# Optimization experiments

Hardware: AMD Instinct MI355X
Metric: run time of the kernel (lower is better)

The kernel has to match this reference:

```python
import jax, jax.numpy as jnp
import numpy as np

B, N, K, H, Cin, Cout = 2, 8192, 16, 4, 64, 128
D = Cout // H  # head_dim = 32


def setup_inputs() -> dict:
    key = jax.random.key(0)
    ks = jax.random.split(key, 16)
    x = jax.random.normal(ks[0], (B, N, Cin), jnp.float32)
    pos = jax.random.uniform(ks[1], (B, N, 3), jnp.float32)
    # KNN indices (torch.no_grad in original): pairwise squared distance + top_k
    sq = jnp.sum(pos * pos, -1)
    d2 = sq[:, :, None] - 2.0 * jnp.einsum('bnc,bmc->bnm', pos, pos) + sq[:, None, :]
    _, idx = jax.lax.top_k(-d2, K)  # (B, N, K) int32

    def lin(k, fin, fout):
        kw, kb = jax.random.split(k)
        lim = 1.0 / np.sqrt(fin)
        W = jax.random.uniform(kw, (fin, fout), jnp.float32, -lim, lim)
        b = jax.random.uniform(kb, (fout,), jnp.float32, -lim, lim)
        return W, b

    Wq, bq = lin(ks[2], Cin, Cout)
    Wkv, bkv = lin(ks[3], Cin, 2 * Cout)
    Wp1, bp1 = lin(ks[4], 3, Cout)
    Wp2, bp2 = lin(ks[5], Cout, Cout)
    Wa1, ba1 = lin(ks[6], Cout, Cout)
    Wa2, ba2 = lin(ks[7], Cout, Cout)
    Wo, bo = lin(ks[8], Cout, Cout)
    return dict(x=x, pos=pos, idx=idx, Wq=Wq, bq=bq, Wkv=Wkv, bkv=bkv,
                Wp1=Wp1, bp1=bp1, Wp2=Wp2, bp2=bp2,
                Wa1=Wa1, ba1=ba1, Wa2=Wa2, ba2=ba2, Wo=Wo, bo=bo)


def reference(x, pos, idx, Wq, bq, Wkv, bkv, Wp1, bp1, Wp2, bp2,
              Wa1, ba1, Wa2, ba2, Wo, bo):
    q = (x @ Wq + bq).reshape(B, N, H, D)
    kv = x @ Wkv + bkv
    k, v = kv[..., :Cout].reshape(B, N, H, D), kv[..., Cout:].reshape(B, N, H, D)
    bix = jnp.arange(B)[:, None, None]
    pos_n = pos[bix, idx]          # (B,N,K,3)
    k_n = k[bix, idx]              # (B,N,K,H,D)
    v_n = v[bix, idx]              # (B,N,K,H,D)
    pos_diff = pos[:, :, None, :] - pos_n
    pos_enc = jax.nn.relu(pos_diff @ Wp1 + bp1) @ Wp2 + bp2   # (B,N,K,Cout)
    pos_enc_h = pos_enc.reshape(B, N, K, H, D)
    rel = (k_n - q[:, :, None] + pos_enc_h).reshape(B, N, K, Cout)
    attn = jax.nn.relu(rel @ Wa1 + ba1) @ Wa2 + ba2           # (B,N,K,Cout)
    attn = jax.nn.softmax(attn.reshape(B, N, K, H, D), axis=2)
    agg = jnp.sum(attn * (v_n + pos_enc_h), axis=2).reshape(B, N, Cout)
    return agg @ Wo + bo
```

## Files before the change

kernel.cpp:

```cpp
#include <hip/hip_runtime.h>
#include <stdint.h>


typedef __attribute__((ext_vector_type(8))) short short8;
typedef __attribute__((ext_vector_type(4))) float f32x4;
typedef __attribute__((ext_vector_type(4))) unsigned int u32x4;

#define NN_TOT 16384
#define PES 136

__device__ __forceinline__ uint32_t pk_bf16(float a, float b) {
  uint32_t r;
  asm("v_cvt_pk_bf16_f32 %0, %1, %2" : "=v"(r) : "v"(a), "v"(b));
  return r;
}
__device__ __forceinline__ float lo_f(uint32_t p) {
  return __builtin_bit_cast(float, p << 16);
}
__device__ __forceinline__ float hi_f(uint32_t p) {
  return __builtin_bit_cast(float, p & 0xffff0000u);
}
__device__ __forceinline__ short f2bf_rne(float f) {
  uint32_t u = __builtin_bit_cast(uint32_t, f);
  uint32_t r = (u + 0x7FFFu + ((u >> 16) & 1u)) >> 16;
  return (short)r;
}
__device__ __forceinline__ float bf2f(unsigned short s) {
  uint32_t u = ((uint32_t)s) << 16;
  return __builtin_bit_cast(float, u);
}

__global__ __launch_bounds__(256) void prep_frags(
    const float* __restrict__ Wq, const float* __restrict__ Wkv,
    const float* __restrict__ Wp2, const float* __restrict__ Wa1,
    const float* __restrict__ Wa2, const float* __restrict__ Wo,
    short* __restrict__ fqh, short* __restrict__ fql,
    short* __restrict__ fwp2, short* __restrict__ fwa1, short* __restrict__ fwa2,
    short* __restrict__ fwoh, short* __restrict__ fwol) {
  int r = blockIdx.x * 256 + threadIdx.x;
  if (r < 3072) {
    int t = r >> 7, rem = r & 127, s = rem >> 6, lane = rem & 63;
    int quad = lane >> 4, l15 = lane & 15;
    int col = t * 16 + l15;
    #pragma unroll
    for (int j = 0; j < 8; j++) {
      int i = 32 * s + quad * 8 + j;
      float wv = (col < 128) ? Wq[i * 128 + col] : Wkv[i * 256 + (col - 128)];
      short hi = f2bf_rne(wv);
      fqh[r * 8 + j] = hi;
      fql[r * 8 + j] = f2bf_rne(wv - bf2f((unsigned short)hi));
    }
  } else {
    int r2 = r - 3072;
    int mat = r2 >> 11;
    int rr = r2 & 2047;
    int t = rr >> 8, rem = rr & 255, s = rem >> 6, lane = rem & 63;
    int quad = lane >> 4, l15 = lane & 15;
    int col = t * 16 + l15;
    const float* W = (mat == 0) ? Wp2 : (mat == 1) ? Wa1 : (mat == 2) ? Wa2 : Wo;
    #pragma unroll
    for (int j = 0; j < 8; j++) {
      int i = 32 * s + quad * 8 + j;
      float wv = W[i * 128 + col];
      short hi = f2bf_rne(wv);
      if (mat == 3) {
        fwoh[rr * 8 + j] = hi;
        fwol[rr * 8 + j] = f2bf_rne(wv - bf2f((unsigned short)hi));
      } else if (mat == 0) fwp2[rr * 8 + j] = hi;
      else if (mat == 1)   fwa1[rr * 8 + j] = hi;
      else                 fwa2[rr * 8 + j] = hi;
    }
  }
}

__device__ __forceinline__ void split_frag(const f32x4 x0, const f32x4 x1,
                                           short8& ah, short8& al) {
  uint32_t h01 = pk_bf16(x0[0], x0[1]);
  uint32_t h23 = pk_bf16(x0[2], x0[3]);
  uint32_t h45 = pk_bf16(x1[0], x1[1]);
  uint32_t h67 = pk_bf16(x1[2], x1[3]);
  u32x4 hh = {h01, h23, h45, h67};
  ah = __builtin_bit_cast(short8, hh);
  uint32_t l01 = pk_bf16(x0[0] - lo_f(h01), x0[1] - hi_f(h01));
  uint32_t l23 = pk_bf16(x0[2] - lo_f(h23), x0[3] - hi_f(h23));
  uint32_t l45 = pk_bf16(x1[0] - lo_f(h45), x1[1] - hi_f(h45));
  uint32_t l67 = pk_bf16(x1[2] - lo_f(h67), x1[3] - hi_f(h67));
  u32x4 ll = {l01, l23, l45, l67};
  al = __builtin_bit_cast(short8, ll);
}

__global__ __launch_bounds__(256) void qkv_kernel(
    const float* __restrict__ x, const float* __restrict__ bq,
    const float* __restrict__ bkv,
    const short* __restrict__ fqh, const short* __restrict__ fql,
    float* __restrict__ q, unsigned short* __restrict__ ko,
    unsigned short* __restrict__ vo) {
  __shared__ __align__(16) short sBq[16384];
  const int tid = threadIdx.x;
  const int sec = blockIdx.x >> 8;
  const int gq = blockIdx.x & 255;
  const int w = tid >> 6, lane = tid & 63;
  const int quad = lane >> 4, l15 = lane & 15;

  {
    const u32x4* sh = reinterpret_cast<const u32x4*>(fqh + sec * 8192);
    const u32x4* sl = reinterpret_cast<const u32x4*>(fql + sec * 8192);
    u32x4* dh = reinterpret_cast<u32x4*>(sBq);
    u32x4* dl = reinterpret_cast<u32x4*>(sBq + 8192);
    #pragma unroll
    for (int i = 0; i < 4; i++) {
      dh[tid + i * 256] = sh[tid + i * 256];
      dl[tid + i * 256] = sl[tid + i * 256];
    }
  }

  const int base = (gq * 4 + w) * 16;
  short8 ah[2], al[2];
  #pragma unroll
  for (int s = 0; s < 2; s++) {
    const float* xp = x + (base + l15) * 64 + 32 * s + quad * 8;
    split_frag(*reinterpret_cast<const f32x4*>(xp),
               *reinterpret_cast<const f32x4*>(xp + 4), ah[s], al[s]);
  }
  __syncthreads();

  #pragma unroll
  for (int tt = 0; tt < 8; tt++) {
    f32x4 acc = {0.f, 0.f, 0.f, 0.f};
    #pragma unroll
    for (int s = 0; s < 2; s++) {
      int rt = tt * 2 + s;
      short8 bh = *reinterpret_cast<const short8*>(sBq + rt * 512 + lane * 8);
      short8 bl = *reinterpret_cast<const short8*>(sBq + 8192 + rt * 512 + lane * 8);
      acc = __builtin_amdgcn_mfma_f32_16x16x32_bf16(ah[s], bh, acc, 0, 0, 0);
      acc = __builtin_amdgcn_mfma_f32_16x16x32_bf16(ah[s], bl, acc, 0, 0, 0);
      acc = __builtin_amdgcn_mfma_f32_16x16x32_bf16(al[s], bh, acc, 0, 0, 0);
    }
    int cl = tt * 16 + l15;
    if (sec == 0) {
      float bias = bq[cl];
      #pragma unroll
      for (int r = 0; r < 4; r++)
        q[(base + quad * 4 + r) * 128 + cl] = acc[r] + bias;
    } else {
      float bias = bkv[(sec - 1) * 128 + cl];
      unsigned short* dst = (sec == 1) ? ko : vo;
      #pragma unroll
      for (int r = 0; r < 4; r++) {
        float vv = acc[r] + bias;
        dst[(base + quad * 4 + r) * 128 + cl] = (unsigned short)pk_bf16(vv, vv);
      }
    }
  }
}

__global__ __launch_bounds__(512, 4) void fused_attn_wo(
    const float* __restrict__ pos, const int* __restrict__ idx,
    const float* __restrict__ Wp1, const float* __restrict__ bp1,
    const float* __restrict__ bp2, const float* __restrict__ ba1,
    const float* __restrict__ ba2,
    const short* __restrict__ fwp2, const short* __restrict__ fwa1,
    const short* __restrict__ fwa2,
    const short* __restrict__ fwoh, const short* __restrict__ fwol,
    const float* __restrict__ bo,
    const float* __restrict__ qg, const unsigned short* __restrict__ kg,
    const unsigned short* __restrict__ vg, float* __restrict__ out) {
  __shared__ __align__(16) short sB[16384];
  __shared__ __align__(16) unsigned short stg[8][16 * PES];
  __shared__ float spd[8][2][16][3];
  __shared__ int sidx[8][2][16];
  float (*sagg)[132] = reinterpret_cast<float(*)[132]>(&stg[0][0]);

  const int tid = threadIdx.x;
  const int w = tid >> 6;
  const int lane = tid & 63;
  const int quad = lane >> 4, l15 = lane & 15;
  const int nb0 = blockIdx.x * 16;
  const int nbw = nb0 + w * 2;

  if (lane < 32) {
    int nn2 = lane >> 4, m = lane & 15;
    int node = nbw + nn2;
    int ji = idx[node * 16 + m];
    int jn = ((node >> 13) << 13) + ji;
    sidx[w][nn2][m] = jn;
    spd[w][nn2][m][0] = pos[node * 3 + 0] - pos[jn * 3 + 0];
    spd[w][nn2][m][1] = pos[node * 3 + 1] - pos[jn * 3 + 1];
    spd[w][nn2][m][2] = pos[node * 3 + 2] - pos[jn * 3 + 2];
  }

  {
    const u32x4* s4 = reinterpret_cast<const u32x4*>(fwp2);
    u32x4* d4 = reinterpret_cast<u32x4*>(sB);
    #pragma unroll
    for (int i = 0; i < 4; i++) d4[tid + i * 512] = s4[tid + i * 512];
  }

  short8 aP[2][4];
  {
    const int c0 = lane, c1 = lane + 64;
    float wp00 = Wp1[c0], wp01 = Wp1[128 + c0], wp02 = Wp1[256 + c0], bb0 = bp1[c0];
    float wp10 = Wp1[c1], wp11 = Wp1[128 + c1], wp12 = Wp1[256 + c1], bb1 = bp1[c1];
    #pragma unroll
    for (int nn2 = 0; nn2 < 2; nn2++) {
      #pragma unroll
      for (int m = 0; m < 16; m++) {
        float d0 = spd[w][nn2][m][0], d1 = spd[w][nn2][m][1], d2 = spd[w][nn2][m][2];
        float h0 = fmaxf(bb0 + d0 * wp00 + d1 * wp01 + d2 * wp02, 0.f);
        float h1 = fmaxf(bb1 + d0 * wp10 + d1 * wp11 + d2 * wp12, 0.f);
        uint32_t pck = pk_bf16(h0, h1);
        stg[w][m * PES + c0] = (unsigned short)pck;
        stg[w][m * PES + c1] = (unsigned short)(pck >> 16);
      }
      #pragma unroll
      for (int s = 0; s < 4; s++)
        aP[nn2][s] = *reinterpret_cast<const short8*>(&stg[w][l15 * PES + 32 * s + quad * 8]);
    }
  }
  __syncthreads();

  short8 k_pk[2][4];
  #pragma unroll
  for (int nn2 = 0; nn2 < 2; nn2++) {
    const unsigned short* kp = kg + sidx[w][nn2][l15] * 128;
    #pragma unroll
    for (int s = 0; s < 4; s++)
      k_pk[nn2][s] = *reinterpret_cast<const short8*>(kp + 32 * s + quad * 8);
  }

  f32x4 acc0[8], acc1[8];

  #pragma unroll
  for (int t = 0; t < 8; t++) { acc0[t] = (f32x4){0,0,0,0}; acc1[t] = (f32x4){0,0,0,0}; }
  #pragma unroll
  for (int s = 0; s < 4; s++) {
    #pragma unroll
    for (int t = 0; t < 8; t++) {
      short8 bf = *reinterpret_cast<const short8*>(sB + ((t * 4 + s) * 64 + lane) * 8);
      acc0[t] = __builtin_amdgcn_mfma_f32_16x16x32_bf16(aP[0][s], bf, acc0[t], 0, 0, 0);
      acc1[t] = __builtin_amdgcn_mfma_f32_16x16x32_bf16(aP[1][s], bf, acc1[t], 0, 0, 0);
    }
  }
  __syncthreads();

  {
    const u32x4* s4 = reinterpret_cast<const u32x4*>(fwa1);
    u32x4* d4 = reinterpret_cast<u32x4*>(sB);
    #pragma unroll
    for (int i = 0; i < 4; i++) d4[tid + i * 512] = s4[tid + i * 512];
  }

  uint32_t pe_pk[2][8][2];
  short8 a2[2][4];
  #pragma unroll
  for (int nn2 = 0; nn2 < 2; nn2++) {
    f32x4* ac = nn2 ? acc1 : acc0;
    const float* qrow = qg + (nbw + nn2) * 128;
    #pragma unroll
    for (int t = 0; t < 8; t++) {
      int c = 16 * t + l15;
      float bb = bp2[c];
      float qv = qrow[c];
      float f0 = ac[t][0] + bb, f1 = ac[t][1] + bb;
      float f2 = ac[t][2] + bb, f3 = ac[t][3] + bb;
      pe_pk[nn2][t][0] = pk_bf16(f0, f1);
      pe_pk[nn2][t][1] = pk_bf16(f2, f3);
      uint32_t g01 = pk_bf16(f0 - qv, f1 - qv);
      uint32_t g23 = pk_bf16(f2 - qv, f3 - qv);
      stg[w][(quad * 4 + 0) * PES + c] = (unsigned short)g01;
      stg[w][(quad * 4 + 1) * PES + c] = (unsigned short)(g01 >> 16);
      stg[w][(quad * 4 + 2) * PES + c] = (unsigned short)g23;
      stg[w][(quad * 4 + 3) * PES + c] = (unsigned short)(g23 >> 16);
    }
    #pragma unroll
    for (int s = 0; s < 4; s++) {
      short8 pq = *reinterpret_cast<const short8*>(&stg[w][l15 * PES + 32 * s + quad * 8]);
      short8 kk = k_pk[nn2][s];
      u32x4 av = {pk_bf16(bf2f((unsigned short)kk[0]) + bf2f((unsigned short)pq[0]),
                          bf2f((unsigned short)kk[1]) + bf2f((unsigned short)pq[1])),
                  pk_bf16(bf2f((unsigned short)kk[2]) + bf2f((unsigned short)pq[2]),
                          bf2f((unsigned short)kk[3]) + bf2f((unsigned short)pq[3])),
                  pk_bf16(bf2f((unsigned short)kk[4]) + bf2f((unsigned short)pq[4]),
                          bf2f((unsigned short)kk[5]) + bf2f((unsigned short)pq[5])),
                  pk_bf16(bf2f((unsigned short)kk[6]) + bf2f((unsigned short)pq[6]),
                          bf2f((unsigned short)kk[7]) + bf2f((unsigned short)pq[7]))};
      a2[nn2][s] = __builtin_bit_cast(short8, av);
    }
  }
  __syncthreads();

  #pragma unroll
  for (int t = 0; t < 8; t++) { acc0[t] = (f32x4){0,0,0,0}; acc1[t] = (f32x4){0,0,0,0}; }
  #pragma unroll
  for (int s = 0; s < 4; s++) {
    #pragma unroll
    for (int t = 0; t < 8; t++) {
      short8 bf = *reinterpret_cast<const short8*>(sB + ((t * 4 + s) * 64 + lane) * 8);
      acc0[t] = __builtin_amdgcn_mfma_f32_16x16x32_bf16(a2[0][s], bf, acc0[t], 0, 0, 0);
      acc1[t] = __builtin_amdgcn_mfma_f32_16x16x32_bf16(a2[1][s], bf, acc1[t], 0, 0, 0);
    }
  }
  __syncthreads();

  {
    const u32x4* s4 = reinterpret_cast<const u32x4*>(fwa2);
    u32x4* d4 = reinterpret_cast<u32x4*>(sB);
    #pragma unroll
    for (int i = 0; i < 4; i++) d4[tid + i * 512] = s4[tid + i * 512];
  }

  short8 a3[2][4];
  #pragma unroll
  for (int nn2 = 0; nn2 < 2; nn2++) {
    f32x4* ac = nn2 ? acc1 : acc0;
    #pragma unroll
    for (int t = 0; t < 8; t++) {
      int c = 16 * t + l15;
      float bb = ba1[c];
      uint32_t p01 = pk_bf16(fmaxf(ac[t][0] + bb, 0.f), fmaxf(ac[t][1] + bb, 0.f));
      uint32_t p23 = pk_bf16(fmaxf(ac[t][2] + bb, 0.f), fmaxf(ac[t][3] + bb, 0.f));
      stg[w][(quad * 4 + 0) * PES + c] = (unsigned short)p01;
      stg[w][(quad * 4 + 1) * PES + c] = (unsigned short)(p01 >> 16);
      stg[w][(quad * 4 + 2) * PES + c] = (unsigned short)p23;
      stg[w][(quad * 4 + 3) * PES + c] = (unsigned short)(p23 >> 16);
    }
    #pragma unroll
    for (int s = 0; s < 4; s++)
      a3[nn2][s] = *reinterpret_cast<const short8*>(&stg[w][l15 * PES + 32 * s + quad * 8]);
  }
  __syncthreads();

  #pragma unroll
  for (int t = 0; t < 8; t++) { acc0[t] = (f32x4){0,0,0,0}; acc1[t] = (f32x4){0,0,0,0}; }
  #pragma unroll
  for (int s = 0; s < 4; s++) {
    #pragma unroll
    for (int t = 0; t < 8; t++) {
      short8 bf = *reinterpret_cast<const short8*>(sB + ((t * 4 + s) * 64 + lane) * 8);
      acc0[t] = __builtin_amdgcn_mfma_f32_16x16x32_bf16(a3[0][s], bf, acc0[t], 0, 0, 0);
      acc1[t] = __builtin_amdgcn_mfma_f32_16x16x32_bf16(a3[1][s], bf, acc1[t], 0, 0, 0);
    }
  }

  int vb[2][4];
  #pragma unroll
  for (int nn2 = 0; nn2 < 2; nn2++)
    #pragma unroll
    for (int r = 0; r < 4; r++)
      vb[nn2][r] = sidx[w][nn2][quad * 4 + r] * 128;

  #pragma unroll
  for (int t = 0; t < 8; t++) {
    int c = 16 * t + l15;
    float bb = ba2[c];
    #pragma unroll
    for (int nn2 = 0; nn2 < 2; nn2++) {
      f32x4* ac = nn2 ? acc1 : acc0;
      float g0 = ac[t][0] + bb, g1 = ac[t][1] + bb;
      float g2 = ac[t][2] + bb, g3 = ac[t][3] + bb;
      float mx = fmaxf(fmaxf(g0, g1), fmaxf(g2, g3));
      mx = fmaxf(mx, __shfl_xor(mx, 16));
      mx = fmaxf(mx, __shfl_xor(mx, 32));
      float e0 = __expf(g0 - mx), e1 = __expf(g1 - mx);
      float e2 = __expf(g2 - mx), e3 = __expf(g3 - mx);
      float ls = e0 + e1 + e2 + e3;
      ls += __shfl_xor(ls, 16);
      ls += __shfl_xor(ls, 32);
      float pe0 = lo_f(pe_pk[nn2][t][0]), pe1 = hi_f(pe_pk[nn2][t][0]);
      float pe2 = lo_f(pe_pk[nn2][t][1]), pe3 = hi_f(pe_pk[nn2][t][1]);
      float p = e0 * (bf2f(vg[vb[nn2][0] + c]) + pe0)
              + e1 * (bf2f(vg[vb[nn2][1] + c]) + pe1)
              + e2 * (bf2f(vg[vb[nn2][2] + c]) + pe2)
              + e3 * (bf2f(vg[vb[nn2][3] + c]) + pe3);
      p += __shfl_xor(p, 16);
      p += __shfl_xor(p, 32);
      if (quad == 0) sagg[w * 2 + nn2][c] = p * __builtin_amdgcn_rcpf(ls);
    }
  }
  __syncthreads();

  {
    short8 ah[4], al[4];
    #pragma unroll
    for (int s = 0; s < 4; s++) {
      f32x4 x0 = *reinterpret_cast<const f32x4*>(&sagg[l15][32 * s + quad * 8]);
      f32x4 x1 = *reinterpret_cast<const f32x4*>(&sagg[l15][32 * s + quad * 8 + 4]);
      split_frag(x0, x1, ah[s], al[s]);
    }
    f32x4 aw = {0.f, 0.f, 0.f, 0.f};
    #pragma unroll
    for (int s = 0; s < 4; s++) {
      short8 bh = *reinterpret_cast<const short8*>(fwoh + ((w * 4 + s) * 64 + lane) * 8);
      short8 bl = *reinterpret_cast<const short8*>(fwol + ((w * 4 + s) * 64 + lane) * 8);
      aw = __builtin_amdgcn_mfma_f32_16x16x32_bf16(ah[s], bh, aw, 0, 0, 0);
      aw = __builtin_amdgcn_mfma_f32_16x16x32_bf16(ah[s], bl, aw, 0, 0, 0);
      aw = __builtin_amdgcn_mfma_f32_16x16x32_bf16(al[s], bh, aw, 0, 0, 0);
    }
    int c = 16 * w + l15;
    float bb = bo[c];
    #pragma unroll
    for (int r = 0; r < 4; r++)
      out[(nb0 + quad * 4 + r) * 128 + c] = aw[r] + bb;
  }
}

extern "C" void kernel_launch(void* const* d_in, const int* in_sizes, int n_in,
                              void* d_out, int out_size, void* d_ws, size_t ws_size,
                              hipStream_t stream) {
  const float* x   = (const float*)d_in[0];
  const float* pos = (const float*)d_in[1];
  const int*   idx = (const int*)d_in[2];
  const float* Wq  = (const float*)d_in[3];
  const float* bq  = (const float*)d_in[4];
  const float* Wkv = (const float*)d_in[5];
  const float* bkv = (const float*)d_in[6];
  const float* Wp1 = (const float*)d_in[7];
  const float* bp1 = (const float*)d_in[8];
  const float* Wp2 = (const float*)d_in[9];
  const float* bp2 = (const float*)d_in[10];
  const float* Wa1 = (const float*)d_in[11];
  const float* ba1 = (const float*)d_in[12];
  const float* Wa2 = (const float*)d_in[13];
  const float* ba2 = (const float*)d_in[14];
  const float* Wo  = (const float*)d_in[15];
  const float* bo  = (const float*)d_in[16];

  char* ws = (char*)d_ws;
  short* fqh  = (short*)(ws + 0);
  short* fql  = (short*)(ws + 49152);
  short* fwp2 = (short*)(ws + 98304);
  short* fwa1 = (short*)(ws + 131072);
  short* fwa2 = (short*)(ws + 163840);
  short* fwoh = (short*)(ws + 196608);
  short* fwol = (short*)(ws + 229376);
  float* qb = (float*)(ws + 262144);
  unsigned short* kb = (unsigned short*)(ws + 262144 + 8388608);
  unsigned short* vb = kb + NN_TOT * 128;

  prep_frags<<<44, 256, 0, stream>>>(Wq, Wkv, Wp2, Wa1, Wa2, Wo,
                                     fqh, fql, fwp2, fwa1, fwa2, fwoh, fwol);
  qkv_kernel<<<768, 256, 0, stream>>>(x, bq, bkv, fqh, fql, qb, kb, vb);
  fused_attn_wo<<<1024, 512, 0, stream>>>(pos, idx, Wp1, bp1, bp2, ba1, ba2,
                                          fwp2, fwa1, fwa2, fwoh, fwol, bo,
                                          qb, kb, vb, (float*)d_out);
}
```

Baseline: 187.1 us.

## Process one node per wave instead of two in fused attention kernel

Each wave now handles a single query node rather than two, so every block covers 8 nodes and the grid doubles to 2048 blocks. Accumulators and fragment arrays are halved, which cuts register pressure and may allow more waves in flight. The cost is that each block still stages all three 128x128 weight matrices into shared memory, so weight staging per node doubles. The final Wo MFMA still computes 16 rows, and half of that work is discarded through a quad<2 guard on the store.

```diff
diff --git a/kernel.cpp b/kernel.cpp
--- a/kernel.cpp
+++ b/kernel.cpp
@@ -167,26 +167,24 @@
     const unsigned short* __restrict__ vg, float* __restrict__ out) {
   __shared__ __align__(16) short sB[16384];
   __shared__ __align__(16) unsigned short stg[8][16 * PES];
-  __shared__ float spd[8][2][16][3];
-  __shared__ int sidx[8][2][16];
+  __shared__ float spd[8][16][3];
+  __shared__ int sidx[8][16];
   float (*sagg)[132] = reinterpret_cast<float(*)[132]>(&stg[0][0]);
 
   const int tid = threadIdx.x;
   const int w = tid >> 6;
   const int lane = tid & 63;
   const int quad = lane >> 4, l15 = lane & 15;
-  const int nb0 = blockIdx.x * 16;
-  const int nbw = nb0 + w * 2;
-
-  if (lane < 32) {
-    int nn2 = lane >> 4, m = lane & 15;
-    int node = nbw + nn2;
-    int ji = idx[node * 16 + m];
+  const int nb0 = blockIdx.x * 8;
+  const int node = nb0 + w;
+
+  if (lane < 16) {
+    int ji = idx[node * 16 + lane];
     int jn = ((node >> 13) << 13) + ji;
-    sidx[w][nn2][m] = jn;
-    spd[w][nn2][m][0] = pos[node * 3 + 0] - pos[jn * 3 + 0];
-    spd[w][nn2][m][1] = pos[node * 3 + 1] - pos[jn * 3 + 1];
-    spd[w][nn2][m][2] = pos[node * 3 + 2] - pos[jn * 3 + 2];
+    sidx[w][lane] = jn;
+    spd[w][lane][0] = pos[node * 3 + 0] - pos[jn * 3 + 0];
+    spd[w][lane][1] = pos[node * 3 + 1] - pos[jn * 3 + 1];
+    spd[w][lane][2] = pos[node * 3 + 2] - pos[jn * 3 + 2];
   }
 
   {
@@ -196,49 +194,44 @@
     for (int i = 0; i < 4; i++) d4[tid + i * 512] = s4[tid + i * 512];
   }
 
-  short8 aP[2][4];
+  short8 aP[4];
   {
     const int c0 = lane, c1 = lane + 64;
     float wp00 = Wp1[c0], wp01 = Wp1[128 + c0], wp02 = Wp1[256 + c0], bb0 = bp1[c0];
     float wp10 = Wp1[c1], wp11 = Wp1[128 + c1], wp12 = Wp1[256 + c1], bb1 = bp1[c1];
     #pragma unroll
-    for (int nn2 = 0; nn2 < 2; nn2++) {
-      #pragma unroll
-      for (int m = 0; m < 16; m++) {
-        float d0 = spd[w][nn2][m][0], d1 = spd[w][nn2][m][1], d2 = spd[w][nn2][m][2];
-        float h0 = fmaxf(bb0 + d0 * wp00 + d1 * wp01 + d2 * wp02, 0.f);
-        float h1 = fmaxf(bb1 + d0 * wp10 + d1 * wp11 + d2 * wp12, 0.f);
-        uint32_t pck = pk_bf16(h0, h1);
-        stg[w][m * PES + c0] = (unsigned short)pck;
-        stg[w][m * PES + c1] = (unsigned short)(pck >> 16);
-      }
-      #pragma unroll
-      for (int s = 0; s < 4; s++)
-        aP[nn2][s] = *reinterpret_cast<const short8*>(&stg[w][l15 * PES + 32 * s + quad * 8]);
-    }
-  }
-  __syncthreads();
-
-  short8 k_pk[2][4];
-  #pragma unroll
-  for (int nn2 = 0; nn2 < 2; nn2++) {
-    const unsigned short* kp = kg + sidx[w][nn2][l15] * 128;
+    for (int m = 0; m < 16; m++) {
+      float d0 = spd[w][m][0], d1 = spd[w][m][1], d2 = spd[w][m][2];
+      float h0 = fmaxf(bb0 + d0 * wp00 + d1 * wp01 + d2 * wp02, 0.f);
+      float h1 = fmaxf(bb1 + d0 * wp10 + d1 * wp11 + d2 * wp12, 0.f);
+      uint32_t pck = pk_bf16(h0, h1);
+      stg[w][m * PES + c0] = (unsigned short)pck;
+      stg[w][m * PES + c1] = (unsigned short)(pck >> 16);
+    }
     #pragma unroll
     for (int s = 0; s < 4; s++)
-      k_pk[nn2][s] = *reinterpret_cast<const short8*>(kp + 32 * s + quad * 8);
-  }
-
-  f32x4 acc0[8], acc1[8];
-
-  #pragma unroll
-  for (int t = 0; t < 8; t++) { acc0[t] = (f32x4){0,0,0,0}; acc1[t] = (f32x4){0,0,0,0}; }
+      aP[s] = *reinterpret_cast<const short8*>(&stg[w][l15 * PES + 32 * s + quad * 8]);
+  }
+  __syncthreads();
+
+  short8 k_pk[4];
+  {
+    const unsigned short* kp = kg + sidx[w][l15] * 128;
+    #pragma unroll
+    for (int s = 0; s < 4; s++)
+      k_pk[s] = *reinterpret_cast<const short8*>(kp + 32 * s + quad * 8);
+  }
+
+  f32x4 acc[8];
+
+  #pragma unroll
+  for (int t = 0; t < 8; t++) acc[t] = (f32x4){0.f, 0.f, 0.f, 0.f};
   #pragma unroll
   for (int s = 0; s < 4; s++) {
     #pragma unroll
     for (int t = 0; t < 8; t++) {
       short8 bf = *reinterpret_cast<const short8*>(sB + ((t * 4 + s) * 64 + lane) * 8);
-      acc0[t] = __builtin_amdgcn_mfma_f32_16x16x32_bf16(aP[0][s], bf, acc0[t], 0, 0, 0);
-      acc1[t] = __builtin_amdgcn_mfma_f32_16x16x32_bf16(aP[1][s], bf, acc1[t], 0, 0, 0);
+      acc[t] = __builtin_amdgcn_mfma_f32_16x16x32_bf16(aP[s], bf, acc[t], 0, 0, 0);
     }
   }
   __syncthreads();
@@ -250,21 +243,19 @@
     for (int i = 0; i < 4; i++) d4[tid + i * 512] = s4[tid + i * 512];
   }
 
-  uint32_t pe_pk[2][8][2];
-  short8 a2[2][4];
-  #pragma unroll
-  for (int nn2 = 0; nn2 < 2; nn2++) {
-    f32x4* ac = nn2 ? acc1 : acc0;
-    const float* qrow = qg + (nbw + nn2) * 128;
+  uint32_t pe_pk[8][2];
+  short8 a2[4];
+  {
+    const float* qrow = qg + node * 128;
     #pragma unroll
     for (int t = 0; t < 8; t++) {
       int c = 16 * t + l15;
       float bb = bp2[c];
       float qv = qrow[c];
-      float f0 = ac[t][0] + bb, f1 = ac[t][1] + bb;
-      float f2 = ac[t][2] + bb, f3 = ac[t][3] + bb;
-      pe_pk[nn2][t][0] = pk_bf16(f0, f1);
-      pe_pk[nn2][t][1] = pk_bf16(f2, f3);
+      float f0 = acc[t][0] + bb, f1 = acc[t][1] + bb;
+      float f2 = acc[t][2] + bb, f3 = acc[t][3] + bb;
+      pe_pk[t][0] = pk_bf16(f0, f1);
+      pe_pk[t][1] = pk_bf16(f2, f3);
       uint32_t g01 = pk_bf16(f0 - qv, f1 - qv);
       uint32_t g23 = pk_bf16(f2 - qv, f3 - qv);
       stg[w][(quad * 4 + 0) * PES + c] = (unsigned short)g01;
@@ -275,7 +266,7 @@
     #pragma unroll
     for (int s = 0; s < 4; s++) {
       short8 pq = *reinterpret_cast<const short8*>(&stg[w][l15 * PES + 32 * s + quad * 8]);
-      short8 kk = k_pk[nn2][s];
+      short8 kk = k_pk[s];
       u32x4 av = {pk_bf16(bf2f((unsigned short)kk[0]) + bf2f((unsigned short)pq[0]),
                           bf2f((unsigned short)kk[1]) + bf2f((unsigned short)pq[1])),
                   pk_bf16(bf2f((unsigned short)kk[2]) + bf2f((unsigned short)pq[2]),
@@ -284,20 +275,19 @@
                           bf2f((unsigned short)kk[5]) + bf2f((unsigned short)pq[5])),
                   pk_bf16(bf2f((unsigned short)kk[6]) + bf2f((unsigned short)pq[6]),
                           bf2f((unsigned short)kk[7]) + bf2f((unsigned short)pq[7]))};
-      a2[nn2][s] = __builtin_bit_cast(short8, av);
-    }
-  }
-  __syncthreads();
-
-  #pragma unroll
-  for (int t = 0; t < 8; t++) { acc0[t] = (f32x4){0,0,0,0}; acc1[t] = (f32x4){0,0,0,0}; }
+      a2[s] = __builtin_bit_cast(short8, av);
+    }
+  }
+  __syncthreads();
+
+  #pragma unroll
+  for (int t = 0; t < 8; t++) acc[t] = (f32x4){0.f, 0.f, 0.f, 0.f};
   #pragma unroll
   for (int s = 0; s < 4; s++) {
     #pragma unroll
     for (int t = 0; t < 8; t++) {
       short8 bf = *reinterpret_cast<const short8*>(sB + ((t * 4 + s) * 64 + lane) * 8);
-      acc0[t] = __builtin_amdgcn_mfma_f32_16x16x32_bf16(a2[0][s], bf, acc0[t], 0, 0, 0);
-      acc1[t] = __builtin_amdgcn_mfma_f32_16x16x32_bf16(a2[1][s], bf, acc1[t], 0, 0, 0);
+      acc[t] = __builtin_amdgcn_mfma_f32_16x16x32_bf16(a2[s], bf, acc[t], 0, 0, 0);
     }
   }
   __syncthreads();
@@ -309,16 +299,14 @@
     for (int i = 0; i < 4; i++) d4[tid + i * 512] = s4[tid + i * 512];
   }
 
-  short8 a3[2][4];
-  #pragma unroll
-  for (int nn2 = 0; nn2 < 2; nn2++) {
-    f32x4* ac = nn2 ? acc1 : acc0;
+  short8 a3[4];
+  {
     #pragma unroll
     for (int t = 0; t < 8; t++) {
       int c = 16 * t + l15;
       float bb = ba1[c];
-      uint32_t p01 = pk_bf16(fmaxf(ac[t][0] + bb, 0.f), fmaxf(ac[t][1] + bb, 0.f));
-      uint32_t p23 = pk_bf16(fmaxf(ac[t][2] + bb, 0.f), fmaxf(ac[t][3] + bb, 0.f));
+      uint32_t p01 = pk_bf16(fmaxf(acc[t][0] + bb, 0.f), fmaxf(acc[t][1] + bb, 0.f));
+      uint32_t p23 = pk_bf16(fmaxf(acc[t][2] + bb, 0.f), fmaxf(acc[t][3] + bb, 0.f));
       stg[w][(quad * 4 + 0) * PES + c] = (unsigned short)p01;
       stg[w][(quad * 4 + 1) * PES + c] = (unsigned short)(p01 >> 16);
       stg[w][(quad * 4 + 2) * PES + c] = (unsigned short)p23;
@@ -326,56 +314,48 @@
     }
     #pragma unroll
     for (int s = 0; s < 4; s++)
-      a3[nn2][s] = *reinterpret_cast<const short8*>(&stg[w][l15 * PES + 32 * s + quad * 8]);
-  }
-  __syncthreads();
-
-  #pragma unroll
-  for (int t = 0; t < 8; t++) { acc0[t] = (f32x4){0,0,0,0}; acc1[t] = (f32x4){0,0,0,0}; }
+      a3[s] = *reinterpret_cast<const short8*>(&stg[w][l15 * PES + 32 * s + quad * 8]);
+  }
+  __syncthreads();
+
+  #pragma unroll
+  for (int t = 0; t < 8; t++) acc[t] = (f32x4){0.f, 0.f, 0.f, 0.f};
   #pragma unroll
   for (int s = 0; s < 4; s++) {
     #pragma unroll
     for (int t = 0; t < 8; t++) {
       short8 bf = *reinterpret_cast<const short8*>(sB + ((t * 4 + s) * 64 + lane) * 8);
-      acc0[t] = __builtin_amdgcn_mfma_f32_16x16x32_bf16(a3[0][s], bf, acc0[t], 0, 0, 0);
-      acc1[t] = __builtin_amdgcn_mfma_f32_16x16x32_bf16(a3[1][s], bf, acc1[t], 0, 0, 0);
-    }
-  }
-
-  int vb[2][4];
-  #pragma unroll
-  for (int nn2 = 0; nn2 < 2; nn2++)
-    #pragma unroll
-    for (int r = 0; r < 4; r++)
-      vb[nn2][r] = sidx[w][nn2][quad * 4 + r] * 128;
+      acc[t] = __builtin_amdgcn_mfma_f32_16x16x32_bf16(a3[s], bf, acc[t], 0, 0, 0);
+    }
+  }
+
+  int vb[4];
+  #pragma unroll
+  for (int r = 0; r < 4; r++) vb[r] = sidx[w][quad * 4 + r] * 128;
 
   #pragma unroll
   for (int t = 0; t < 8; t++) {
     int c = 16 * t + l15;
     float bb = ba2[c];
-    #pragma unroll
-    for (int nn2 = 0; nn2 < 2; nn2++) {
-      f32x4* ac = nn2 ? acc1 : acc0;
-      float g0 = ac[t][0] + bb, g1 = ac[t][1] + bb;
-      float g2 = ac[t][2] + bb, g3 = ac[t][3] + bb;
-      float mx = fmaxf(fmaxf(g0, g1), fmaxf(g2, g3));
-      mx = fmaxf(mx, __shfl_xor(mx, 16));
-      mx = fmaxf(mx, __shfl_xor(mx, 32));
-      float e0 = __expf(g0 - mx), e1 = __expf(g1 - mx);
-      float e2 = __expf(g2 - mx), e3 = __expf(g3 - mx);
-      float ls = e0 + e1 + e2 + e3;
-      ls += __shfl_xor(ls, 16);
-      ls += __shfl_xor(ls, 32);
-      float pe0 = lo_f(pe_pk[nn2][t][0]), pe1 = hi_f(pe_pk[nn2][t][0]);
-      float pe2 = lo_f(pe_pk[nn2][t][1]), pe3 = hi_f(pe_pk[nn2][t][1]);
-      float p = e0 * (bf2f(vg[vb[nn2][0] + c]) + pe0)
-              + e1 * (bf2f(vg[vb[nn2][1] + c]) + pe1)
-              + e2 * (bf2f(vg[vb[nn2][2] + c]) + pe2)
-              + e3 * (bf2f(vg[vb[nn2][3] + c]) + pe3);
-      p += __shfl_xor(p, 16);
-      p += __shfl_xor(p, 32);
-      if (quad == 0) sagg[w * 2 + nn2][c] = p * __builtin_amdgcn_rcpf(ls);
-    }
+    float g0 = acc[t][0] + bb, g1 = acc[t][1] + bb;
+    float g2 = acc[t][2] + bb, g3 = acc[t][3] + bb;
+    float mx = fmaxf(fmaxf(g0, g1), fmaxf(g2, g3));
+    mx = fmaxf(mx, __shfl_xor(mx, 16));
+    mx = fmaxf(mx, __shfl_xor(mx, 32));
+    float e0 = __expf(g0 - mx), e1 = __expf(g1 - mx);
+    float e2 = __expf(g2 - mx), e3 = __expf(g3 - mx);
+    float ls = e0 + e1 + e2 + e3;
+    ls += __shfl_xor(ls, 16);
+    ls += __shfl_xor(ls, 32);
+    float pe0 = lo_f(pe_pk[t][0]), pe1 = hi_f(pe_pk[t][0]);
+    float pe2 = lo_f(pe_pk[t][1]), pe3 = hi_f(pe_pk[t][1]);
+    float p = e0 * (bf2f(vg[vb[0] + c]) + pe0)
+            + e1 * (bf2f(vg[vb[1] + c]) + pe1)
+            + e2 * (bf2f(vg[vb[2] + c]) + pe2)
+            + e3 * (bf2f(vg[vb[3] + c]) + pe3);
+    p += __shfl_xor(p, 16);
+    p += __shfl_xor(p, 32);
+    if (quad == 0) sagg[w][c] = p * __builtin_amdgcn_rcpf(ls);
   }
   __syncthreads();
 
@@ -398,9 +378,11 @@
     }
     int c = 16 * w + l15;
     float bb = bo[c];
-    #pragma unroll
-    for (int r = 0; r < 4; r++)
-      out[(nb0 + quad * 4 + r) * 128 + c] = aw[r] + bb;
+    if (quad < 2) {
+      #pragma unroll
+      for (int r = 0; r < 4; r++)
+        out[(nb0 + quad * 4 + r) * 128 + c] = aw[r] + bb;
+    }
   }
 }
 
@@ -440,7 +422,7 @@
   prep_frags<<<44, 256, 0, stream>>>(Wq, Wkv, Wp2, Wa1, Wa2, Wo,
                                      fqh, fql, fwp2, fwa1, fwa2, fwoh, fwol);
   qkv_kernel<<<768, 256, 0, stream>>>(x, bq, bkv, fqh, fql, qb, kb, vb);
-  fused_attn_wo<<<1024, 512, 0, stream>>>(pos, idx, Wp1, bp1, bp2, ba1, ba2,
+  fused_attn_wo<<<2048, 512, 0, stream>>>(pos, idx, Wp1, bp1, bp2, ba1, ba2,
                                           fwp2, fwa1, fwa2, fwoh, fwol, bo,
                                           qb, kb, vb, (float*)d_out);
 }
```

Result: faster. 177.9 us (-4.9%).
